# Performance work log

Measured on AMD Instinct MI355X. Metric: run time of the kernel, lower is better.

## Reference

```python
import jax, jax.numpy as jnp
import numpy as np
from jax import lax

MAX_U = 5
MAX_V = 5
BN_EPS = 1e-5


def _conv(x, w, b, p):
    # NCHW conv with symmetric padding p (torch Conv2d padding=p)
    y = lax.conv_general_dilated(x, w, (1, 1), [(p, p), (p, p)],
                                 dimension_numbers=('NCHW', 'OIHW', 'NCHW'))
    return y + b[None, :, None, None]


def _branch(x, w3, b3, w5, b5, w7, b7):
    a3 = jax.nn.relu(_conv(x, w3, b3, 1))
    a5 = jax.nn.relu(_conv(jnp.concatenate([a3, x], 1), w5, b5, 2))
    a7 = jax.nn.relu(_conv(jnp.concatenate([a5, x], 1), w7, b7, 3))
    return jnp.concatenate([a3, a5, a7], 1)  # [B, 448, H, W]


def _dct_basis(n, kmax, dtype):
    # orthonormal DCT-II basis rows for frequencies u < kmax: [kmax, n]
    i = jnp.arange(n, dtype=dtype)
    u = jnp.arange(kmax, dtype=dtype)
    basis = jnp.cos(jnp.pi * (2.0 * i[None, :] + 1.0) * u[:, None] / (2.0 * n))
    scale = jnp.where(u == 0, jnp.sqrt(1.0 / n), jnp.sqrt(2.0 / n))
    return basis * scale[:, None]


def setup_inputs() -> dict:
    key = jax.random.key(0)
    ks = iter(jax.random.split(key, 64))

    def w(shape, s=0.05):
        return (jax.random.normal(next(ks), shape, jnp.float32) * s)

    cin = 3  # input_channels per group (x has 2*cin = 6 channels)
    inp = {"x": jax.random.normal(next(ks), (16, 6, 64, 64), jnp.float32)}
    for g in (1, 2):
        for b in (1, 2):
            inp[f"g{g}b{b}c3_w"] = w((64, cin, 3, 3))
            inp[f"g{g}b{b}c3_b"] = w((64,))
            inp[f"g{g}b{b}c5_w"] = w((128, 64 + cin, 5, 5))
            inp[f"g{g}b{b}c5_b"] = w((128,))
            inp[f"g{g}b{b}c7_w"] = w((256, 128 + cin, 7, 7))
            inp[f"g{g}b{b}c7_b"] = w((256,))
    inp["gap_w"] = w((12, 1792)); inp["gap_b"] = w((12,))
    inp["dct_w"] = w((12, 1792)); inp["dct_b"] = w((12,))
    inp["bn_gamma"] = jnp.ones((1792,), jnp.float32)
    inp["bn_beta"] = jnp.zeros((1792,), jnp.float32)
    inp["bn_mean"] = jnp.zeros((1792,), jnp.float32)
    inp["bn_var"] = jnp.ones((1792,), jnp.float32)
    return inp


def reference(x,
              g1b1c3_w, g1b1c3_b, g1b1c5_w, g1b1c5_b, g1b1c7_w, g1b1c7_b,
              g1b2c3_w, g1b2c3_b, g1b2c5_w, g1b2c5_b, g1b2c7_w, g1b2c7_b,
              g2b1c3_w, g2b1c3_b, g2b1c5_w, g2b1c5_b, g2b1c7_w, g2b1c7_b,
              g2b2c3_w, g2b2c3_b, g2b2c5_w, g2b2c5_b, g2b2c7_w, g2b2c7_b,
              gap_w, gap_b, dct_w, dct_b, bn_gamma, bn_beta, bn_mean, bn_var):
    B, C, H, W = x.shape  # C is even (6)
    half = C // 2
    x1, x2 = x[:, :half], x[:, half:]
    out1 = jnp.concatenate([
        _branch(x1, g1b1c3_w, g1b1c3_b, g1b1c5_w, g1b1c5_b, g1b1c7_w, g1b1c7_b),
        _branch(x1, g1b2c3_w, g1b2c3_b, g1b2c5_w, g1b2c5_b, g1b2c7_w, g1b2c7_b)], 1)
    out2 = jnp.concatenate([
        _branch(x2, g2b1c3_w, g2b1c3_b, g2b1c5_w, g2b1c5_b, g2b1c7_w, g2b1c7_b),
        _branch(x2, g2b2c3_w, g2b2c3_b, g2b2c5_w, g2b2c5_b, g2b2c7_w, g2b2c7_b)], 1)
    concat_out = jnp.concatenate([out1, out2], 1)  # [B, 1792, H, W]

    # GAP head
    gap = concat_out.mean((2, 3))  # [B, 1792]
    gap_pred = gap @ gap_w.T + gap_b

    # Batched multi-frequency DCT compression: low-frequency 5x5 block of the
    # 2D DCT-II of each channel, averaged -> one scalar per channel.
    Bh = _dct_basis(H, MAX_U, x.dtype)  # [5, H]
    Bw = _dct_basis(W, MAX_V, x.dtype)  # [5, W]
    coeff = jnp.einsum('bchw,uh,vw->bcuv', concat_out, Bh, Bw)  # [B,1792,5,5]
    dct_feat = coeff.mean((2, 3))  # [B, 1792]

    # BatchNorm1d (inference with running stats); dropout is identity in eval.
    bn = bn_gamma * (dct_feat - bn_mean) / jnp.sqrt(bn_var + BN_EPS) + bn_beta
    dct_pred = bn @ dct_w.T + dct_b
    return gap_pred, dct_pred
```

## Files before the change

### kernel.cpp

```cpp
#include <hip/hip_runtime.h>
#include <hip/hip_bf16.h>
#include <math.h>

#define HW 64
#define NPIX 4096
#define NB 16
#define NCH 1792
#define PW 72
#define PROWS 70
#define PLANE (PROWS * PW)

typedef __bf16 bf16;
typedef __bf16 bf16x8 __attribute__((ext_vector_type(8)));
typedef float f32x4 __attribute__((ext_vector_type(4)));

struct PtrQuad { const float* p[4]; };

constexpr size_t W3SZ = 9 * 1 * 64 * 32;
constexpr size_t W5SZ = 25 * 3 * 128 * 32;
constexpr size_t W7SZ = 49 * 5 * 256 * 32;
constexpr size_t WBR  = W3SZ + W5SZ + W7SZ;
constexpr size_t PLE  = (size_t)PLANE * 8;

__global__ __launch_bounds__(256) void init_kernel(float* __restrict__ gap_sum,
                                                   float* __restrict__ dct_sum,
                                                   float* __restrict__ dctw) {
    int tid = blockIdx.x * 256 + threadIdx.x;
    if (tid < NB * NCH) { gap_sum[tid] = 0.f; dct_sum[tid] = 0.f; }
    if (blockIdx.x == 0 && threadIdx.x < HW) {
        int i = threadIdx.x;
        float s = 0.f;
        for (int u = 0; u < 5; ++u) {
            float scale = (u == 0) ? 0.125f : 0.17677669529663687f;
            s += cosf(3.14159265358979323846f * (2.f * i + 1.f) * u / 128.f) * scale;
        }
        dctw[i] = s * 0.2f;
    }
}

__global__ __launch_bounds__(256) void zero_kernel(float4* __restrict__ p, long n) {
    long i = (long)blockIdx.x * 256 + threadIdx.x;
    long stride = (long)gridDim.x * 256;
    for (; i < n; i += stride) p[i] = float4{0.f, 0.f, 0.f, 0.f};
}

__global__ __launch_bounds__(256) void prep_x_kernel(const float* __restrict__ x,
                                                     bf16* __restrict__ xp) {
    int tid = blockIdx.x * 256 + threadIdx.x;
    if (tid >= NB * 2 * NPIX) return;
    int pix = tid & (NPIX - 1);
    int g = (tid >> 12) & 1;
    int b = tid >> 13;
    int h = pix >> 6, w = pix & 63;
    size_t base = ((size_t)(b * 2 + g) * 4) * PLE + ((size_t)(h + 3) * PW + (w + 3)) * 8;
    for (int c = 0; c < 3; ++c)
        xp[base + c] = (bf16)x[((size_t)(b * 6 + g * 3 + c)) * NPIX + pix];
}

template <int K, int CHUNKS, int CIN_ACT, int COUT>
__global__ __launch_bounds__(256) void prep_w_all(PtrQuad src, bf16* __restrict__ dst) {
    constexpr int CIN = CIN_ACT + 3;
    constexpr int TOT = K * K * CHUNKS * COUT * 32;
    int tid = blockIdx.x * 256 + threadIdx.x;
    if (tid >= 4 * TOT) return;
    int br = tid / TOT;
    int idx = tid - br * TOT;
    int cc = idx & 31;
    int co = (idx >> 5) % COUT;
    int rest = idx / (32 * COUT);
    int chunk = rest % CHUNKS;
    int ks = rest / CHUNKS;
    int ky = ks / K, kx = ks % K;
    int ci;
    if (chunk < CHUNKS - 1) ci = chunk * 32 + cc;
    else ci = (cc < 3) ? (CIN_ACT + cc) : -1;
    const float* w = src.p[br];
    float v = (ci >= 0) ? w[(((size_t)co * CIN + ci) * K + ky) * K + kx] : 0.f;
    dst[(size_t)br * WBR + idx] = (bf16)v;
}

template <int K, int CHUNKS, int COUT, int NBLK, bool STORE>
__global__ __launch_bounds__(256, 2) void conv_mfma(
    const bf16* __restrict__ act_in,
    const bf16* __restrict__ xpad,
    const bf16* __restrict__ wall, size_t stage_woff,
    PtrQuad biasq,
    bf16* __restrict__ act_out,
    float* __restrict__ gap_sum, float* __restrict__ dct_sum,
    int stage_coff, const float* __restrict__ dctw, int br0,
    int br_mask, int br_bits)
{
    constexpr int PAD = K / 2;
    constexpr int COFF = 3 - PAD;
    constexpr int HR = 4 + K - 1;
    constexpr int UN = HR * PW;
    constexpr int NI = (UN + 63) / 64;
    constexpr int ACT_CHUNKS = CHUNKS - 1;
    constexpr int WN = NBLK / 32;
    constexpr int CW = CHUNKS * COUT * 32;
    constexpr int OPL = COUT / 8;

    __shared__ __align__(16) bf16 s_in[4 * HR * PW * 8];

    const int tid = threadIdx.x;
    const int lane = tid & 63;
    const int wv = tid >> 6;
    const int wavem = wv >> 1;
    const int wn = wv & 1;
    const int q = lane >> 4;
    const int ln = lane & 15;

    const int bx = blockIdx.x;
    const int lbr = bx & br_mask;
    const int row = bx >> br_bits;
    const int b = blockIdx.z;
    const int br = br0 + lbr;
    const int g = br >> 1;

    const int o0 = row * 4;
    const int prow0 = o0 + COFF;
    const int n0 = blockIdx.y * NBLK + wn * (NBLK / 2);

    const bf16* wrep = wall + (size_t)br * WBR + stage_woff;
    const float* bias = biasq.p[br];
    const size_t img = (size_t)(lbr * NB + b);

    int abase[8];
#pragma unroll
    for (int t = 0; t < 8; ++t) {
        int lr = wavem * 2 + (t >> 2);
        int ct = (t & 3) * 16;
        abase[t] = ((q * HR + lr) * PW + ct + ln + COFF) * 8;
    }

    f32x4 acc[8][WN];
#pragma unroll
    for (int t = 0; t < 8; ++t)
#pragma unroll
        for (int u = 0; u < WN; ++u) acc[t][u] = f32x4{0.f, 0.f, 0.f, 0.f};

    const bf16* xsrc = xpad + ((size_t)((b * 2 + g) * 4 + wv)) * PLE;

#pragma unroll 1
    for (int chunk = 0; chunk < CHUNKS; ++chunk) {
        __syncthreads();
        {
            const bf16* pl = (chunk < ACT_CHUNKS)
                ? act_in + (img * (ACT_CHUNKS * 4) + chunk * 4 + wv) * PLE
                : xsrc;
            const bf16* gb = pl + (size_t)prow0 * PW * 8;
            bf16* lb = s_in + (size_t)wv * HR * PW * 8;
#pragma unroll
            for (int i = 0; i < NI; ++i) {
                int u = i * 64 + lane;
                if (UN % 64 == 0 || u < UN)
                    __builtin_amdgcn_global_load_lds(
                        (const __attribute__((address_space(1))) void*)(gb + (size_t)u * 8),
                        (__attribute__((address_space(3))) void*)(lb + i * 512),
                        16, 0, 0);
            }
        }
        __syncthreads();

        const bf16* wchunk = wrep + ((size_t)chunk * COUT + n0) * 32 + ln * 32 + q * 8;

#pragma unroll 1
        for (int ky = 0; ky < K; ++ky) {
            const int kyoff = ky * PW * 8;
#pragma unroll
            for (int kx = 0; kx < K; ++kx) {
                const bf16* wstep = wchunk + (size_t)(ky * K + kx) * CW;
                bf16x8 bfr[WN];
#pragma unroll
                for (int u = 0; u < WN; ++u)
                    bfr[u] = *(const bf16x8*)(wstep + u * 512);
                const int koff = kyoff + kx * 8;
                bf16x8 afr[8];
#pragma unroll
                for (int t = 0; t < 8; ++t)
                    afr[t] = *(const bf16x8*)(s_in + abase[t] + koff);
#pragma unroll
                for (int t = 0; t < 8; ++t)
#pragma unroll
                    for (int u = 0; u < WN; ++u)
                        acc[t][u] = __builtin_amdgcn_mfma_f32_16x16x32_bf16(
                            afr[t], bfr[u], acc[t][u], 0, 0, 0);
            }
        }
    }

    float gsum[WN], dsum[WN], bv[WN];
#pragma unroll
    for (int u = 0; u < WN; ++u) {
        gsum[u] = 0.f; dsum[u] = 0.f;
        bv[u] = bias[n0 + u * 16 + ln];
    }

#pragma unroll
    for (int t = 0; t < 8; ++t) {
        const int lr = wavem * 2 + (t >> 2);
        const int gr = o0 + lr;
        const float wrow = dctw[gr];
        const int ct = (t & 3) * 16;
#pragma unroll
        for (int r = 0; r < 4; ++r) {
            const int gc = ct + q * 4 + r;
            const float wcd = dctw[gc] * wrow;
#pragma unroll
            for (int u = 0; u < WN; ++u) {
                float v = fmaxf(acc[t][u][r] + bv[u], 0.f);
                if constexpr (STORE) {
                    int ch = n0 + u * 16 + ln;
                    act_out[(img * OPL + (ch >> 3)) * PLE +
                            ((size_t)(gr + 3) * PW + (gc + 3)) * 8 + (ch & 7)] = (bf16)v;
                }
                gsum[u] += v;
                dsum[u] = fmaf(v, wcd, dsum[u]);
            }
        }
    }

    const int cb = br * 448 + stage_coff;
#pragma unroll
    for (int u = 0; u < WN; ++u) {
        float gv = gsum[u], dv = dsum[u];
        gv += __shfl_xor(gv, 16, 64); gv += __shfl_xor(gv, 32, 64);
        dv += __shfl_xor(dv, 16, 64); dv += __shfl_xor(dv, 32, 64);
        if (q == 0) {
            int ch = cb + n0 + u * 16 + ln;
            atomicAdd(&gap_sum[b * NCH + ch], gv);
            atomicAdd(&dct_sum[b * NCH + ch], dv);
        }
    }
}

__global__ __launch_bounds__(256) void head_kernel(
    const float* __restrict__ gap_sum, const float* __restrict__ dct_sum,
    const float* __restrict__ gap_w, const float* __restrict__ gap_b,
    const float* __restrict__ dct_w, const float* __restrict__ dct_b,
    const float* __restrict__ gamma, const float* __restrict__ beta,
    const float* __restrict__ mean, const float* __restrict__ var,
    float* __restrict__ out)
{
    const int blk = blockIdx.x;
    const int b = blk / 24;
    const int rem = blk - b * 24;
    const int kind = rem / 12;
    const int i = rem - kind * 12;
    const int tid = threadIdx.x;

    float partial = 0.f;
    if (kind == 0) {
        for (int cc = tid; cc < NCH; cc += 256)
            partial += gap_sum[b * NCH + cc] * (1.f / 4096.f) * gap_w[i * NCH + cc];
    } else {
        for (int cc = tid; cc < NCH; cc += 256) {
            float f = dct_sum[b * NCH + cc];
            f = gamma[cc] * (f - mean[cc]) * rsqrtf(var[cc] + 1e-5f) + beta[cc];
            partial += f * dct_w[i * NCH + cc];
        }
    }
#pragma unroll
    for (int off = 32; off > 0; off >>= 1) partial += __shfl_down(partial, off, 64);
    __shared__ float red[4];
    if ((tid & 63) == 0) red[tid >> 6] = partial;
    __syncthreads();
    if (tid == 0) {
        float tot = red[0] + red[1] + red[2] + red[3];
        tot += (kind == 0 ? gap_b[i] : dct_b[i]);
        out[kind * (NB * 12) + b * 12 + i] = tot;
    }
}

extern "C" void kernel_launch(void* const* d_in, const int* in_sizes, int n_in,
                              void* d_out, int out_size, void* d_ws, size_t ws_size,
                              hipStream_t stream)
{
    const float* x = (const float*)d_in[0];

    float* fws = (float*)d_ws;
    float* dctw    = fws;
    float* gap_sum = fws + 64;
    float* dct_sum = gap_sum + NB * NCH;
    bf16* bws = (bf16*)(dct_sum + NB * NCH);

    const size_t WALL_E = 4 * WBR;
    const size_t XP_E   = (size_t)NB * 2 * 4 * PLE;
    const size_t A3_BR  = (size_t)NB * 8 * PLE;
    const size_t A5_BR  = (size_t)NB * 16 * PLE;

    const size_t fixed_b = 229632 + 2 * (WALL_E + XP_E);
    int nbr = 1, br_bits = 0;
    if (ws_size >= fixed_b + 2 * 4 * (A3_BR + A5_BR)) { nbr = 4; br_bits = 2; }
    else if (ws_size >= fixed_b + 2 * 2 * (A3_BR + A5_BR)) { nbr = 2; br_bits = 1; }
    const int br_mask = nbr - 1;

    bf16* wall = bws;
    bf16* xp   = wall + WALL_E;
    bf16* a3p  = xp + XP_E;
    bf16* a5p  = a3p + (size_t)nbr * A3_BR;

    hipLaunchKernelGGL(init_kernel, dim3((NB * NCH + 255) / 256), dim3(256), 0, stream,
                       gap_sum, dct_sum, dctw);

    const long zero16 = (long)((XP_E + (size_t)nbr * (A3_BR + A5_BR)) * 2 / 16);
    hipLaunchKernelGGL(zero_kernel, dim3(2048), dim3(256), 0, stream, (float4*)xp, zero16);

    hipLaunchKernelGGL(prep_x_kernel, dim3((NB * 2 * NPIX) / 256), dim3(256), 0, stream, x, xp);

    PtrQuad w3q = {{(const float*)d_in[1], (const float*)d_in[7], (const float*)d_in[13], (const float*)d_in[19]}};
    PtrQuad b3q = {{(const float*)d_in[2], (const float*)d_in[8], (const float*)d_in[14], (const float*)d_in[20]}};
    PtrQuad w5q = {{(const float*)d_in[3], (const float*)d_in[9], (const float*)d_in[15], (const float*)d_in[21]}};
    PtrQuad b5q = {{(const float*)d_in[4], (const float*)d_in[10], (const float*)d_in[16], (const float*)d_in[22]}};
    PtrQuad w7q = {{(const float*)d_in[5], (const float*)d_in[11], (const float*)d_in[17], (const float*)d_in[23]}};
    PtrQuad b7q = {{(const float*)d_in[6], (const float*)d_in[12], (const float*)d_in[18], (const float*)d_in[24]}};

    hipLaunchKernelGGL((prep_w_all<3, 1, 0, 64>), dim3((4 * W3SZ + 255) / 256), dim3(256), 0, stream, w3q, wall);
    hipLaunchKernelGGL((prep_w_all<5, 3, 64, 128>), dim3((4 * W5SZ + 255) / 256), dim3(256), 0, stream, w5q, wall + W3SZ);
    hipLaunchKernelGGL((prep_w_all<7, 5, 128, 256>), dim3((4 * W7SZ + 255) / 256), dim3(256), 0, stream, w7q, wall + W3SZ + W5SZ);

    for (int br0 = 0; br0 < 4; br0 += nbr) {
        hipLaunchKernelGGL((conv_mfma<3, 1, 64, 64, true>), dim3(16 * nbr, 1, NB), dim3(256), 0, stream,
                           (const bf16*)nullptr, xp, wall, 0, b3q,
                           a3p, gap_sum, dct_sum, 0, dctw, br0, br_mask, br_bits);
        hipLaunchKernelGGL((conv_mfma<5, 3, 128, 128, true>), dim3(16 * nbr, 1, NB), dim3(256), 0, stream,
                           a3p, xp, wall, W3SZ, b5q,
                           a5p, gap_sum, dct_sum, 64, dctw, br0, br_mask, br_bits);
        hipLaunchKernelGGL((conv_mfma<7, 5, 256, 128, false>), dim3(16 * nbr, 2, NB), dim3(256), 0, stream,
                           a5p, xp, wall, W3SZ + W5SZ, b7q,
                           (bf16*)nullptr, gap_sum, dct_sum, 192, dctw, br0, br_mask, br_bits);
    }

    hipLaunchKernelGGL(head_kernel, dim3(NB * 24), dim3(256), 0, stream,
                       gap_sum, dct_sum,
                       (const float*)d_in[25], (const float*)d_in[26],
                       (const float*)d_in[27], (const float*)d_in[28],
                       (const float*)d_in[29], (const float*)d_in[30],
                       (const float*)d_in[31], (const float*)d_in[32],
                       (float*)d_out);
}
```

Before: 970.7 us.

## Switch conv MFMA from 16x16x32 to 32x32x16 tiles

Reworks the convolution inner loop to use 32x32x16 bf16 MFMA instructions instead of 16x16x32. Each wave now covers 32 output pixels by 32 channels per instruction, and the 32-channel K chunk is split into two 16-wide steps. The LDS fragment indexing, the weight lane mapping and the epilogue element-to-pixel mapping are all rewritten to match. The larger tiles need fewer LDS and weight fragment loads per FLOP, at the cost of a more complex accumulator layout and WN halving, which requires NBLK of at least 64.

After: 1.077 ms. +11.0%, slower.

```diff
diff --git a/kernel.cpp b/kernel.cpp
--- a/kernel.cpp
+++ b/kernel.cpp
@@ -12,7 +12,7 @@
 
 typedef __bf16 bf16;
 typedef __bf16 bf16x8 __attribute__((ext_vector_type(8)));
-typedef float f32x4 __attribute__((ext_vector_type(4)));
+typedef float f32x16 __attribute__((ext_vector_type(16)));
 
 struct PtrQuad { const float* p[4]; };
 
@@ -96,7 +96,7 @@
     constexpr int UN = HR * PW;
     constexpr int NI = (UN + 63) / 64;
     constexpr int ACT_CHUNKS = CHUNKS - 1;
-    constexpr int WN = NBLK / 32;
+    constexpr int WN = NBLK / 64;
     constexpr int CW = CHUNKS * COUT * 32;
     constexpr int OPL = COUT / 8;
 
@@ -107,8 +107,8 @@
     const int wv = tid >> 6;
     const int wavem = wv >> 1;
     const int wn = wv & 1;
-    const int q = lane >> 4;
-    const int ln = lane & 15;
+    const int l5 = lane & 31;
+    const int hb = lane >> 5;
 
     const int bx = blockIdx.x;
     const int lbr = bx & br_mask;
@@ -125,19 +125,23 @@
     const float* bias = biasq.p[br];
     const size_t img = (size_t)(lbr * NB + b);
 
-    int abase[8];
-#pragma unroll
-    for (int t = 0; t < 8; ++t) {
-        int lr = wavem * 2 + (t >> 2);
-        int ct = (t & 3) * 16;
-        abase[t] = ((q * HR + lr) * PW + ct + ln + COFF) * 8;
-    }
-
-    f32x4 acc[8][WN];
-#pragma unroll
-    for (int t = 0; t < 8; ++t)
-#pragma unroll
-        for (int u = 0; u < WN; ++u) acc[t][u] = f32x4{0.f, 0.f, 0.f, 0.f};
+    int base_mt[4];
+#pragma unroll
+    for (int t = 0; t < 4; ++t) {
+        int lr = wavem * 2 + (t >> 1);
+        int ct = (t & 1) * 32;
+        base_mt[t] = (lr * PW + ct + l5 + COFF) * 8;
+    }
+    const int poff[2] = { hb * HR * PW * 8, (2 + hb) * HR * PW * 8 };
+    const int lane_w = l5 * 32 + hb * 8;
+
+    f32x16 acc[4][WN];
+#pragma unroll
+    for (int t = 0; t < 4; ++t)
+#pragma unroll
+        for (int u = 0; u < WN; ++u)
+#pragma unroll
+            for (int r = 0; r < 16; ++r) acc[t][u][r] = 0.f;
 
     const bf16* xsrc = xpad + ((size_t)((b * 2 + g) * 4 + wv)) * PLE;
 
@@ -162,7 +166,7 @@
         }
         __syncthreads();
 
-        const bf16* wchunk = wrep + ((size_t)chunk * COUT + n0) * 32 + ln * 32 + q * 8;
+        const bf16* wchunk = wrep + ((size_t)chunk * COUT + n0) * 32 + lane_w;
 
 #pragma unroll 1
         for (int ky = 0; ky < K; ++ky) {
@@ -170,21 +174,24 @@
 #pragma unroll
             for (int kx = 0; kx < K; ++kx) {
                 const bf16* wstep = wchunk + (size_t)(ky * K + kx) * CW;
-                bf16x8 bfr[WN];
-#pragma unroll
-                for (int u = 0; u < WN; ++u)
-                    bfr[u] = *(const bf16x8*)(wstep + u * 512);
                 const int koff = kyoff + kx * 8;
-                bf16x8 afr[8];
-#pragma unroll
-                for (int t = 0; t < 8; ++t)
-                    afr[t] = *(const bf16x8*)(s_in + abase[t] + koff);
-#pragma unroll
-                for (int t = 0; t < 8; ++t)
+#pragma unroll
+                for (int s = 0; s < 2; ++s) {
+                    bf16x8 bfr[WN];
 #pragma unroll
                     for (int u = 0; u < WN; ++u)
-                        acc[t][u] = __builtin_amdgcn_mfma_f32_16x16x32_bf16(
-                            afr[t], bfr[u], acc[t][u], 0, 0, 0);
+                        bfr[u] = *(const bf16x8*)(wstep + u * 1024 + s * 16);
+                    bf16x8 afr[4];
+#pragma unroll
+                    for (int t = 0; t < 4; ++t)
+                        afr[t] = *(const bf16x8*)(s_in + poff[s] + base_mt[t] + koff);
+#pragma unroll
+                    for (int t = 0; t < 4; ++t)
+#pragma unroll
+                        for (int u = 0; u < WN; ++u)
+                            acc[t][u] = __builtin_amdgcn_mfma_f32_32x32x16_bf16(
+                                afr[t], bfr[u], acc[t][u], 0, 0, 0);
+                }
             }
         }
     }
@@ -193,24 +200,24 @@
 #pragma unroll
     for (int u = 0; u < WN; ++u) {
         gsum[u] = 0.f; dsum[u] = 0.f;
-        bv[u] = bias[n0 + u * 16 + ln];
-    }
-
-#pragma unroll
-    for (int t = 0; t < 8; ++t) {
-        const int lr = wavem * 2 + (t >> 2);
-        const int gr = o0 + lr;
+        bv[u] = bias[n0 + u * 32 + l5];
+    }
+
+#pragma unroll
+    for (int t = 0; t < 4; ++t) {
+        const int gr = o0 + wavem * 2 + (t >> 1);
         const float wrow = dctw[gr];
-        const int ct = (t & 3) * 16;
-#pragma unroll
-        for (int r = 0; r < 4; ++r) {
-            const int gc = ct + q * 4 + r;
+        const int colbase = (t & 1) * 32;
+#pragma unroll
+        for (int r = 0; r < 16; ++r) {
+            const int p = (r & 3) + 8 * (r >> 2) + 4 * hb;
+            const int gc = colbase + p;
             const float wcd = dctw[gc] * wrow;
 #pragma unroll
             for (int u = 0; u < WN; ++u) {
                 float v = fmaxf(acc[t][u][r] + bv[u], 0.f);
                 if constexpr (STORE) {
-                    int ch = n0 + u * 16 + ln;
+                    int ch = n0 + u * 32 + l5;
                     act_out[(img * OPL + (ch >> 3)) * PLE +
                             ((size_t)(gr + 3) * PW + (gc + 3)) * 8 + (ch & 7)] = (bf16)v;
                 }
@@ -224,10 +231,10 @@
 #pragma unroll
     for (int u = 0; u < WN; ++u) {
         float gv = gsum[u], dv = dsum[u];
-        gv += __shfl_xor(gv, 16, 64); gv += __shfl_xor(gv, 32, 64);
-        dv += __shfl_xor(dv, 16, 64); dv += __shfl_xor(dv, 32, 64);
-        if (q == 0) {
-            int ch = cb + n0 + u * 16 + ln;
+        gv += __shfl_xor(gv, 32, 64);
+        dv += __shfl_xor(dv, 32, 64);
+        if (hb == 0) {
+            int ch = cb + n0 + u * 32 + l5;
             atomicAdd(&gap_sum[b * NCH + ch], gv);
             atomicAdd(&dct_sum[b * NCH + ch], dv);
         }
```

## Pack input-channel taps into shared MFMA K slices and zero only halos

Applied to the files above, without the earlier changes.

The 3-channel raw input that each conv concatenates was padded to a whole 32-wide K chunk per filter tap. It is now stored as a single 8-channel plane, and four taps are packed into one MFMA K=32 step, with each lane quad reading a different tap offset. This removes most of the wasted MFMAs and LDS loads for the x chunk. The weight layout is regenerated to match. Full zeroing of the activation buffers is replaced by writing only the halo borders, which cuts memset traffic.

Result: faster. 880.9 us (-9.3%).

```diff
diff --git a/kernel.cpp b/kernel.cpp
--- a/kernel.cpp
+++ b/kernel.cpp
@@ -16,11 +16,14 @@
 
 struct PtrQuad { const float* p[4]; };
 
-constexpr size_t W3SZ = 9 * 1 * 64 * 32;
-constexpr size_t W5SZ = 25 * 3 * 128 * 32;
-constexpr size_t W7SZ = 49 * 5 * 256 * 32;
+constexpr size_t PLE = (size_t)PLANE * 8;
+
+constexpr int nstepx(int K) { return (K * K + 3) / 4; }
+
+constexpr size_t W3SZ = (size_t)nstepx(3) * 64 * 32;
+constexpr size_t W5SZ = (size_t)25 * 2 * 128 * 32 + nstepx(5) * 128 * 32;
+constexpr size_t W7SZ = (size_t)49 * 4 * 256 * 32 + nstepx(7) * 256 * 32;
 constexpr size_t WBR  = W3SZ + W5SZ + W7SZ;
-constexpr size_t PLE  = (size_t)PLANE * 8;
 
 __global__ __launch_bounds__(256) void init_kernel(float* __restrict__ gap_sum,
                                                    float* __restrict__ dct_sum,
@@ -38,10 +41,17 @@
     }
 }
 
-__global__ __launch_bounds__(256) void zero_kernel(float4* __restrict__ p, long n) {
-    long i = (long)blockIdx.x * 256 + threadIdx.x;
-    long stride = (long)gridDim.x * 256;
-    for (; i < n; i += stride) p[i] = float4{0.f, 0.f, 0.f, 0.f};
+__global__ __launch_bounds__(256) void halo_zero(bf16* __restrict__ base, int nplanes) {
+    int tid = blockIdx.x * 256 + threadIdx.x;
+    if (tid >= nplanes * 944) return;
+    int p = tid / 944, u = tid - p * 944;
+    int row, col;
+    if (u < 432) { row = u / PW; col = u - row * PW; if (row >= 3) row += 64; }
+    else { int v = u - 432; row = 3 + (v >> 3); int c = v & 7; col = (c < 3) ? c : 64 + c; }
+    bf16x8 z;
+#pragma unroll
+    for (int j = 0; j < 8; ++j) z[j] = (bf16)0.f;
+    *(bf16x8*)(base + ((size_t)p * PLANE + row * PW + col) * 8) = z;
 }
 
 __global__ __launch_bounds__(256) void prep_x_kernel(const float* __restrict__ x,
@@ -52,34 +62,53 @@
     int g = (tid >> 12) & 1;
     int b = tid >> 13;
     int h = pix >> 6, w = pix & 63;
-    size_t base = ((size_t)(b * 2 + g) * 4) * PLE + ((size_t)(h + 3) * PW + (w + 3)) * 8;
+    bf16x8 v;
+#pragma unroll
+    for (int j = 0; j < 8; ++j) v[j] = (bf16)0.f;
     for (int c = 0; c < 3; ++c)
-        xp[base + c] = (bf16)x[((size_t)(b * 6 + g * 3 + c)) * NPIX + pix];
-}
-
-template <int K, int CHUNKS, int CIN_ACT, int COUT>
+        v[c] = (bf16)x[((size_t)(b * 6 + g * 3 + c)) * NPIX + pix];
+    *(bf16x8*)(xp + ((size_t)(b * 2 + g) * PLANE + (size_t)(h + 3) * PW + (w + 3)) * 8) = v;
+}
+
+template <int K, int ACT_CHUNKS, int CIN_ACT, int COUT>
 __global__ __launch_bounds__(256) void prep_w_all(PtrQuad src, bf16* __restrict__ dst) {
     constexpr int CIN = CIN_ACT + 3;
-    constexpr int TOT = K * K * CHUNKS * COUT * 32;
+    constexpr int KK = K * K;
+    constexpr int NSX = (KK + 3) / 4;
+    constexpr int ACT_TOT = KK * ACT_CHUNKS * COUT * 32;
+    constexpr int X_TOT = NSX * COUT * 32;
+    constexpr int TOT = ACT_TOT + X_TOT;
+    constexpr int ACD = ACT_CHUNKS ? ACT_CHUNKS : 1;
     int tid = blockIdx.x * 256 + threadIdx.x;
     if (tid >= 4 * TOT) return;
     int br = tid / TOT;
     int idx = tid - br * TOT;
-    int cc = idx & 31;
-    int co = (idx >> 5) % COUT;
-    int rest = idx / (32 * COUT);
-    int chunk = rest % CHUNKS;
-    int ks = rest / CHUNKS;
-    int ky = ks / K, kx = ks % K;
-    int ci;
-    if (chunk < CHUNKS - 1) ci = chunk * 32 + cc;
-    else ci = (cc < 3) ? (CIN_ACT + cc) : -1;
     const float* w = src.p[br];
-    float v = (ci >= 0) ? w[(((size_t)co * CIN + ci) * K + ky) * K + kx] : 0.f;
+    float v;
+    if (idx < ACT_TOT) {
+        int cc = idx & 31;
+        int co = (idx >> 5) % COUT;
+        int rest = idx / (32 * COUT);
+        int chunk = rest % ACD;
+        int ks = rest / ACD;
+        int ky = ks / K, kx = ks % K;
+        v = w[(((size_t)co * CIN + chunk * 32 + cc) * K + ky) * K + kx];
+    } else {
+        int xi = idx - ACT_TOT;
+        int j = xi & 7;
+        int slot = (xi >> 3) & 3;
+        int co = (xi >> 5) % COUT;
+        int s = xi / (32 * COUT);
+        int tap = 4 * s + slot;
+        if (tap < KK && j < 3) {
+            int ky = tap / K, kx = tap % K;
+            v = w[(((size_t)co * CIN + CIN_ACT + j) * K + ky) * K + kx];
+        } else v = 0.f;
+    }
     dst[(size_t)br * WBR + idx] = (bf16)v;
 }
 
-template <int K, int CHUNKS, int COUT, int NBLK, bool STORE>
+template <int K, int ACT_CHUNKS, int COUT, int NBLK, bool STORE>
 __global__ __launch_bounds__(256, 2) void conv_mfma(
     const bf16* __restrict__ act_in,
     const bf16* __restrict__ xpad,
@@ -95,9 +124,11 @@
     constexpr int HR = 4 + K - 1;
     constexpr int UN = HR * PW;
     constexpr int NI = (UN + 63) / 64;
-    constexpr int ACT_CHUNKS = CHUNKS - 1;
     constexpr int WN = NBLK / 32;
-    constexpr int CW = CHUNKS * COUT * 32;
+    constexpr int KK = K * K;
+    constexpr int NSX = (KK + 3) / 4;
+    constexpr int CW = ACT_CHUNKS * COUT * 32;
+    constexpr int XOFF = KK * ACT_CHUNKS * COUT * 32;
     constexpr int OPL = COUT / 8;
 
     __shared__ __align__(16) bf16 s_in[4 * HR * PW * 8];
@@ -139,15 +170,11 @@
 #pragma unroll
         for (int u = 0; u < WN; ++u) acc[t][u] = f32x4{0.f, 0.f, 0.f, 0.f};
 
-    const bf16* xsrc = xpad + ((size_t)((b * 2 + g) * 4 + wv)) * PLE;
-
 #pragma unroll 1
-    for (int chunk = 0; chunk < CHUNKS; ++chunk) {
+    for (int chunk = 0; chunk < ACT_CHUNKS; ++chunk) {
         __syncthreads();
         {
-            const bf16* pl = (chunk < ACT_CHUNKS)
-                ? act_in + (img * (ACT_CHUNKS * 4) + chunk * 4 + wv) * PLE
-                : xsrc;
+            const bf16* pl = act_in + (img * (ACT_CHUNKS * 4) + chunk * 4 + wv) * PLE;
             const bf16* gb = pl + (size_t)prow0 * PW * 8;
             bf16* lb = s_in + (size_t)wv * HR * PW * 8;
 #pragma unroll
@@ -186,6 +213,59 @@
                         acc[t][u] = __builtin_amdgcn_mfma_f32_16x16x32_bf16(
                             afr[t], bfr[u], acc[t][u], 0, 0, 0);
             }
+        }
+    }
+
+    __syncthreads();
+    {
+        const bf16* gb = xpad + (size_t)(b * 2 + g) * PLE + (size_t)prow0 * PW * 8;
+        constexpr int PERW = (UN + 3) / 4;
+        const int u0 = wv * PERW;
+        bf16* lb = s_in + (size_t)u0 * 8;
+        constexpr int NIX = (PERW + 63) / 64;
+#pragma unroll
+        for (int i = 0; i < NIX; ++i) {
+            int u = i * 64 + lane;
+            if (u < PERW && u0 + u < UN)
+                __builtin_amdgcn_global_load_lds(
+                    (const __attribute__((address_space(1))) void*)(gb + (size_t)(u0 + u) * 8),
+                    (__attribute__((address_space(3))) void*)(lb + i * 512),
+                    16, 0, 0);
+        }
+    }
+    __syncthreads();
+
+    {
+        int xabase[8];
+#pragma unroll
+        for (int t = 0; t < 8; ++t) {
+            int lr = wavem * 2 + (t >> 2);
+            int ct = (t & 3) * 16;
+            xabase[t] = (lr * PW + ct + ln + COFF) * 8;
+        }
+        const bf16* wx = wrep + XOFF + (size_t)n0 * 32 + ln * 32 + q * 8;
+#pragma unroll
+        for (int s = 0; s < NSX; ++s) {
+            int tap = 4 * s + q;
+            if (tap > KK - 1) tap = KK - 1;
+            int ky = tap / K;
+            int kx = tap - ky * K;
+            int xoff = (ky * PW + kx) * 8;
+            const bf16* ws = wx + (size_t)s * COUT * 32;
+            bf16x8 bfr[WN];
+#pragma unroll
+            for (int u = 0; u < WN; ++u)
+                bfr[u] = *(const bf16x8*)(ws + u * 512);
+            bf16x8 afr[8];
+#pragma unroll
+            for (int t = 0; t < 8; ++t)
+                afr[t] = *(const bf16x8*)(s_in + xabase[t] + xoff);
+#pragma unroll
+            for (int t = 0; t < 8; ++t)
+#pragma unroll
+                for (int u = 0; u < WN; ++u)
+                    acc[t][u] = __builtin_amdgcn_mfma_f32_16x16x32_bf16(
+                        afr[t], bfr[u], acc[t][u], 0, 0, 0);
         }
     }
 
@@ -285,7 +365,7 @@
     bf16* bws = (bf16*)(dct_sum + NB * NCH);
 
     const size_t WALL_E = 4 * WBR;
-    const size_t XP_E   = (size_t)NB * 2 * 4 * PLE;
+    const size_t XP_E   = (size_t)NB * 2 * PLE;
     const size_t A3_BR  = (size_t)NB * 8 * PLE;
     const size_t A5_BR  = (size_t)NB * 16 * PLE;
 
@@ -303,8 +383,9 @@
     hipLaunchKernelGGL(init_kernel, dim3((NB * NCH + 255) / 256), dim3(256), 0, stream,
                        gap_sum, dct_sum, dctw);
 
-    const long zero16 = (long)((XP_E + (size_t)nbr * (A3_BR + A5_BR)) * 2 / 16);
-    hipLaunchKernelGGL(zero_kernel, dim3(2048), dim3(256), 0, stream, (float4*)xp, zero16);
+    const int nplanes = NB * 2 + nbr * NB * (8 + 16);
+    hipLaunchKernelGGL(halo_zero, dim3((nplanes * 944 + 255) / 256), dim3(256), 0, stream,
+                       xp, nplanes);
 
     hipLaunchKernelGGL(prep_x_kernel, dim3((NB * 2 * NPIX) / 256), dim3(256), 0, stream, x, xp);
 
@@ -315,18 +396,21 @@
     PtrQuad w7q = {{(const float*)d_in[5], (const float*)d_in[11], (const float*)d_in[17], (const float*)d_in[23]}};
     PtrQuad b7q = {{(const float*)d_in[6], (const float*)d_in[12], (const float*)d_in[18], (const float*)d_in[24]}};
 
-    hipLaunchKernelGGL((prep_w_all<3, 1, 0, 64>), dim3((4 * W3SZ + 255) / 256), dim3(256), 0, stream, w3q, wall);
-    hipLaunchKernelGGL((prep_w_all<5, 3, 64, 128>), dim3((4 * W5SZ + 255) / 256), dim3(256), 0, stream, w5q, wall + W3SZ);
-    hipLaunchKernelGGL((prep_w_all<7, 5, 128, 256>), dim3((4 * W7SZ + 255) / 256), dim3(256), 0, stream, w7q, wall + W3SZ + W5SZ);
+    hipLaunchKernelGGL((prep_w_all<3, 0, 0, 64>), dim3((4 * W3SZ + 255) / 256), dim3(256), 0, stream,
+                       w3q, wall);
+    hipLaunchKernelGGL((prep_w_all<5, 2, 64, 128>), dim3((4 * W5SZ + 255) / 256), dim3(256), 0, stream,
+                       w5q, wall + W3SZ);
+    hipLaunchKernelGGL((prep_w_all<7, 4, 128, 256>), dim3((4 * W7SZ + 255) / 256), dim3(256), 0, stream,
+                       w7q, wall + W3SZ + W5SZ);
 
     for (int br0 = 0; br0 < 4; br0 += nbr) {
-        hipLaunchKernelGGL((conv_mfma<3, 1, 64, 64, true>), dim3(16 * nbr, 1, NB), dim3(256), 0, stream,
+        hipLaunchKernelGGL((conv_mfma<3, 0, 64, 64, true>), dim3(16 * nbr, 1, NB), dim3(256), 0, stream,
                            (const bf16*)nullptr, xp, wall, 0, b3q,
                            a3p, gap_sum, dct_sum, 0, dctw, br0, br_mask, br_bits);
-        hipLaunchKernelGGL((conv_mfma<5, 3, 128, 128, true>), dim3(16 * nbr, 1, NB), dim3(256), 0, stream,
+        hipLaunchKernelGGL((conv_mfma<5, 2, 128, 128, true>), dim3(16 * nbr, 1, NB), dim3(256), 0, stream,
                            a3p, xp, wall, W3SZ, b5q,
                            a5p, gap_sum, dct_sum, 64, dctw, br0, br_mask, br_bits);
-        hipLaunchKernelGGL((conv_mfma<7, 5, 256, 128, false>), dim3(16 * nbr, 2, NB), dim3(256), 0, stream,
+        hipLaunchKernelGGL((conv_mfma<7, 4, 256, 128, false>), dim3(16 * nbr, 2, NB), dim3(256), 0, stream,
                            a5p, xp, wall, W3SZ + W5SZ, b7q,
                            (bf16*)nullptr, gap_sum, dct_sum, 192, dctw, br0, br_mask, br_bits);
     }
```
